# Optimization experiments

Hardware: AMD Instinct MI355X
Metric: run time of the kernel (lower is better)

Reference implementation:

```python
import jax, jax.numpy as jnp
import numpy as np

N_ITEMS = 100000
N_USERS = 16384
HIST = 50
TEXT_DIM = 256
GCN_DIM = 128
HIDDEN_DIM = 512
TOWER_DIM = 128


def _l2norm(x, eps=1e-12):
    # F.normalize(dim=1): x / max(||x||, eps)
    n = jnp.sqrt(jnp.sum(x * x, axis=1, keepdims=True))
    return x / jnp.maximum(n, eps)


def setup_inputs() -> dict:
    key = jax.random.key(0)
    ks = jax.random.split(key, 10)
    s1i = 1.0 / np.sqrt(TEXT_DIM + GCN_DIM)
    s2i = 1.0 / np.sqrt(HIDDEN_DIM)
    s1u = 1.0 / np.sqrt(GCN_DIM + TOWER_DIM)
    return {
        "item_text_emb": jax.random.normal(ks[0], (N_ITEMS, TEXT_DIM), jnp.float32),
        "gcn_item_emb": jax.random.normal(ks[1], (N_ITEMS, GCN_DIM), jnp.float32),
        "gcn_user_emb": jax.random.normal(ks[2], (N_USERS, GCN_DIM), jnp.float32),
        "hist_idx": jax.random.randint(ks[3], (N_USERS, HIST), 0, N_ITEMS),
        "W1i": jax.random.normal(ks[4], (TEXT_DIM + GCN_DIM, HIDDEN_DIM), jnp.float32) * s1i,
        "b1i": jnp.zeros((HIDDEN_DIM,), jnp.float32),
        "W2i": jax.random.normal(ks[5], (HIDDEN_DIM, TOWER_DIM), jnp.float32) * s2i,
        "b2i": jnp.zeros((TOWER_DIM,), jnp.float32),
        "W1u": jax.random.normal(ks[6], (GCN_DIM + TOWER_DIM, HIDDEN_DIM), jnp.float32) * s1u,
        "b1u": jnp.zeros((HIDDEN_DIM,), jnp.float32),
        "W2u": jax.random.normal(ks[7], (HIDDEN_DIM, TOWER_DIM), jnp.float32) * s2i,
        "b2u": jnp.zeros((TOWER_DIM,), jnp.float32),
    }


def reference(item_text_emb, gcn_item_emb, gcn_user_emb, hist_idx,
              W1i, b1i, W2i, b2i, W1u, b1u, W2u, b2u):
    # encode_items: MLP over concat(text, gcn) features, then L2 normalize
    item_feat = jnp.concatenate([item_text_emb, gcn_item_emb], axis=1)  # [N_items, text+gcn]
    h = jax.nn.relu(item_feat @ W1i + b1i)
    item_emb = _l2norm(h @ W2i + b2i)  # [N_items, TOWER_DIM]
    # encode_users: per-user gather of history item embeddings + mean pooling
    hist = jnp.mean(item_emb[hist_idx], axis=1)  # [N_users, TOWER_DIM]
    fused = jnp.concatenate([gcn_user_emb, hist], axis=1)
    hu = jax.nn.relu(fused @ W1u + b1u)
    user_emb = _l2norm(hu @ W2u + b2u)  # [N_users, TOWER_DIM]
    return user_emb
```

## Files before the change

kernel.cpp:

```cpp
#include <hip/hip_runtime.h>
#include <hip/hip_bf16.h>

#define HIST 50
#define N_ITEMS 100000
#define N_USERS 16384

typedef __bf16 bf8 __attribute__((ext_vector_type(8)));
typedef float  f4  __attribute__((ext_vector_type(4)));

__device__ __forceinline__ unsigned short f2bf(float x) {
    unsigned u = __builtin_bit_cast(unsigned, x);
    u += 0x7fffu + ((u >> 16) & 1u);
    return (unsigned short)(u >> 16);
}
__device__ __forceinline__ float bf2f(unsigned b) {
    unsigned u = b << 16;
    return __builtin_bit_cast(float, u);
}

__global__ void pack_weights(const float* __restrict__ W1i, const float* __restrict__ W2i,
                             const float* __restrict__ W1u, const float* __restrict__ W2u,
                             unsigned short* __restrict__ dstbase)
{
    int i = blockIdx.x * 256 + threadIdx.x;
    const float* W; unsigned short* dst; int N, KS, loc;
    if (i < 24576)      { W = W1i; dst = dstbase;          N = 512; KS = 12; loc = i; }
    else if (i < 32768) { W = W2i; dst = dstbase + 196608; N = 128; KS = 16; loc = i - 24576; }
    else if (i < 49152) { W = W1u; dst = dstbase + 262144; N = 512; KS = 8;  loc = i - 32768; }
    else                { W = W2u; dst = dstbase + 393216; N = 128; KS = 16; loc = i - 49152; }
    int l = loc & 63, fi = loc >> 6;
    int ks = fi % KS, nt = fi / KS;
    int q = l >> 4, c = l & 15;
    const float* src = W + (size_t)(ks * 32 + q * 8) * N + nt * 16 + c;
    unsigned o[4];
    #pragma unroll
    for (int k = 0; k < 4; ++k) {
        unsigned lo = f2bf(src[(2 * k) * N]);
        unsigned hi = f2bf(src[(2 * k + 1) * N]);
        o[k] = lo | (hi << 16);
    }
    uint4 v; v.x = o[0]; v.y = o[1]; v.z = o[2]; v.w = o[3];
    ((uint4*)dst)[(size_t)(nt * KS + ks) * 64 + l] = v;
}

template<int KS1, int ASTR, bool OUT_BF16>
__device__ __forceinline__ void tower_core(
    unsigned short* U, const float* b1s, const float* b2s, float* sumsq,
    const bf8* __restrict__ w1f, const bf8* __restrict__ w2f,
    void* __restrict__ outp, int row0, int tid)
{
    const int HSTR = 520;
    const int l = tid & 63, w = tid >> 6;
    const int q = l >> 4, c = l & 15;

    f4 acc1[2][4];
    #pragma unroll
    for (int i = 0; i < 2; ++i)
        #pragma unroll
        for (int j = 0; j < 4; ++j) acc1[i][j] = (f4)0.0f;

    const unsigned short* ap = U + c * ASTR + q * 8;
    #pragma unroll
    for (int ks = 0; ks < KS1; ++ks) {
        bf8 a0 = *(const bf8*)(ap + ks * 32);
        bf8 a1 = *(const bf8*)(ap + 16 * ASTR + ks * 32);
        #pragma unroll
        for (int nt = 0; nt < 4; ++nt) {
            bf8 b = w1f[(size_t)((w * 4 + nt) * KS1 + ks) * 64 + l];
            acc1[0][nt] = __builtin_amdgcn_mfma_f32_16x16x32_bf16(a0, b, acc1[0][nt], 0, 0, 0);
            acc1[1][nt] = __builtin_amdgcn_mfma_f32_16x16x32_bf16(a1, b, acc1[1][nt], 0, 0, 0);
        }
    }
    __syncthreads();

    #pragma unroll
    for (int nt = 0; nt < 4; ++nt) {
        int col = w * 64 + nt * 16 + c;
        float bias = b1s[col];
        #pragma unroll
        for (int rt = 0; rt < 2; ++rt)
            #pragma unroll
            for (int reg = 0; reg < 4; ++reg) {
                float h = fmaxf(acc1[rt][nt][reg] + bias, 0.0f);
                U[(rt * 16 + q * 4 + reg) * HSTR + col] = f2bf(h);
            }
    }
    __syncthreads();

    const int rg = w >> 2, jj = w & 3;
    f4 acc2[2];
    acc2[0] = (f4)0.0f; acc2[1] = (f4)0.0f;

    const unsigned short* hp = U + (size_t)(rg * 16 + c) * HSTR + q * 8;
    #pragma unroll
    for (int ks = 0; ks < 16; ++ks) {
        bf8 a = *(const bf8*)(hp + ks * 32);
        bf8 b0 = w2f[(size_t)((jj * 2 + 0) * 16 + ks) * 64 + l];
        bf8 b1 = w2f[(size_t)((jj * 2 + 1) * 16 + ks) * 64 + l];
        acc2[0] = __builtin_amdgcn_mfma_f32_16x16x32_bf16(a, b0, acc2[0], 0, 0, 0);
        acc2[1] = __builtin_amdgcn_mfma_f32_16x16x32_bf16(a, b1, acc2[1], 0, 0, 0);
    }

    float v[2][4];
    #pragma unroll
    for (int j = 0; j < 2; ++j) {
        float bias = b2s[jj * 32 + j * 16 + c];
        #pragma unroll
        for (int reg = 0; reg < 4; ++reg)
            v[j][reg] = acc2[j][reg] + bias;
    }
    #pragma unroll
    for (int reg = 0; reg < 4; ++reg) {
        float s = v[0][reg] * v[0][reg] + v[1][reg] * v[1][reg];
        s += __shfl_xor(s, 1); s += __shfl_xor(s, 2);
        s += __shfl_xor(s, 4); s += __shfl_xor(s, 8);
        if (c == 0) atomicAdd(&sumsq[rg * 16 + q * 4 + reg], s);
    }
    __syncthreads();
    #pragma unroll
    for (int reg = 0; reg < 4; ++reg) {
        int row = rg * 16 + q * 4 + reg;
        float inv = 1.0f / fmaxf(sqrtf(sumsq[row]), 1e-12f);
        #pragma unroll
        for (int j = 0; j < 2; ++j) {
            int col = jj * 32 + j * 16 + c;
            float o = v[j][reg] * inv;
            if (OUT_BF16)
                ((unsigned short*)outp)[(size_t)(row0 + row) * 128 + col] = f2bf(o);
            else
                ((float*)outp)[(size_t)(row0 + row) * 128 + col] = o;
        }
    }
}

#define ASI 392
#define ASU 264

__global__ __launch_bounds__(512, 8) void item_kernel(
    const float* __restrict__ text, const float* __restrict__ gcn,
    const bf8* __restrict__ w1f, const float* __restrict__ b1,
    const bf8* __restrict__ w2f, const float* __restrict__ b2,
    unsigned short* __restrict__ item_bf)
{
    __shared__ __align__(16) unsigned short U[32 * 520];
    __shared__ float b1s[512], b2s[128], sumsq[32];
    const int tid = threadIdx.x;
    const int row0 = blockIdx.x * 32;
    const float4* t4 = (const float4*)text;
    const float4* g4 = (const float4*)gcn;
    #pragma unroll
    for (int j = 0; j < 4; ++j) {
        int idx = tid + j * 512; int r = idx >> 6, c4 = idx & 63;
        float4 x = t4[(size_t)(row0 + r) * 64 + c4];
        ushort4 s; s.x = f2bf(x.x); s.y = f2bf(x.y); s.z = f2bf(x.z); s.w = f2bf(x.w);
        *(ushort4*)(U + r * ASI + c4 * 4) = s;
    }
    #pragma unroll
    for (int j = 0; j < 2; ++j) {
        int idx = tid + j * 512; int r = idx >> 5, c4 = idx & 31;
        float4 x = g4[(size_t)(row0 + r) * 32 + c4];
        ushort4 s; s.x = f2bf(x.x); s.y = f2bf(x.y); s.z = f2bf(x.z); s.w = f2bf(x.w);
        *(ushort4*)(U + r * ASI + 256 + c4 * 4) = s;
    }
    b1s[tid] = b1[tid];
    if (tid < 128) b2s[tid] = b2[tid];
    if (tid < 32)  sumsq[tid] = 0.0f;
    __syncthreads();
    tower_core<12, ASI, true>(U, b1s, b2s, sumsq, w1f, w2f, item_bf, row0, tid);
}

__global__ __launch_bounds__(512, 8) void user_kernel(
    const float* __restrict__ gcnu, const int* __restrict__ hist,
    const unsigned short* __restrict__ item_bf,
    const bf8* __restrict__ w1f, const float* __restrict__ b1,
    const bf8* __restrict__ w2f, const float* __restrict__ b2,
    float* __restrict__ outp)
{
    __shared__ __align__(16) unsigned short U[32 * 520];
    __shared__ float b1s[512], b2s[128], sumsq[32];
    const int tid = threadIdx.x;
    const int u0 = blockIdx.x * 32;
    int* hist_s = (int*)(U + 32 * ASU);
    const float4* g4 = (const float4*)gcnu;
    #pragma unroll
    for (int j = 0; j < 2; ++j) {
        int idx = tid + j * 512; int r = idx >> 5, c4 = idx & 31;
        float4 x = g4[(size_t)(u0 + r) * 32 + c4];
        ushort4 s; s.x = f2bf(x.x); s.y = f2bf(x.y); s.z = f2bf(x.z); s.w = f2bf(x.w);
        *(ushort4*)(U + r * ASU + c4 * 4) = s;
    }
    for (int k = tid; k < 32 * HIST; k += 512)
        hist_s[k] = hist[(size_t)u0 * HIST + k];
    b1s[tid] = b1[tid];
    if (tid < 128) b2s[tid] = b2[tid];
    if (tid < 32)  sumsq[tid] = 0.0f;
    __syncthreads();
    {
        const int u = tid >> 4, g = tid & 15;
        float f[8];
        #pragma unroll
        for (int k = 0; k < 8; ++k) f[k] = 0.0f;
        const int* hrow = hist_s + u * HIST;
        #pragma unroll 10
        for (int t = 0; t < HIST; ++t) {
            int id = hrow[t];
            uint4 x = *(const uint4*)(item_bf + (size_t)id * 128 + g * 8);
            unsigned vs[4] = {x.x, x.y, x.z, x.w};
            #pragma unroll
            for (int k = 0; k < 4; ++k) {
                f[2 * k]     += bf2f(vs[k] & 0xffffu);
                f[2 * k + 1] += bf2f(vs[k] >> 16);
            }
        }
        unsigned o[4];
        #pragma unroll
        for (int k = 0; k < 4; ++k)
            o[k] = (unsigned)f2bf(f[2 * k] * 0.02f) | ((unsigned)f2bf(f[2 * k + 1] * 0.02f) << 16);
        uint4 s; s.x = o[0]; s.y = o[1]; s.z = o[2]; s.w = o[3];
        *(uint4*)(U + u * ASU + 128 + g * 8) = s;
    }
    __syncthreads();
    tower_core<8, ASU, false>(U, b1s, b2s, sumsq, w1f, w2f, outp, u0, tid);
}

extern "C" void kernel_launch(void* const* d_in, const int* in_sizes, int n_in,
                              void* d_out, int out_size, void* d_ws, size_t ws_size,
                              hipStream_t stream) {
    const float* text = (const float*)d_in[0];
    const float* gcni = (const float*)d_in[1];
    const float* gcnu = (const float*)d_in[2];
    const int*   hist = (const int*)d_in[3];
    const float* W1i  = (const float*)d_in[4];
    const float* b1i  = (const float*)d_in[5];
    const float* W2i  = (const float*)d_in[6];
    const float* b2i  = (const float*)d_in[7];
    const float* W1u  = (const float*)d_in[8];
    const float* b1u  = (const float*)d_in[9];
    const float* W2u  = (const float*)d_in[10];
    const float* b2u  = (const float*)d_in[11];
    float* out = (float*)d_out;

    unsigned short* itemb = (unsigned short*)d_ws;
    unsigned short* pw = itemb + 12800000;

    pack_weights<<<224, 256, 0, stream>>>(W1i, W2i, W1u, W2u, pw);
    item_kernel<<<N_ITEMS / 32, 512, 0, stream>>>(
        text, gcni, (const bf8*)pw, b1i, (const bf8*)(pw + 196608), b2i, itemb);
    user_kernel<<<N_USERS / 32, 512, 0, stream>>>(
        gcnu, hist, itemb, (const bf8*)(pw + 262144), b1u, (const bf8*)(pw + 393216), b2u, out);
}
```

Before: 320.3 us.

## Double item tile to 64 rows, prefetch weight fragments, use nontemporal loads/stores

The item kernel now processes 64 rows per block instead of 32. Each weight fragment fetched from global memory is reused across four row tiles instead of two, which halves weight traffic per item. Weight fragments for the next k-step are software-prefetched into registers in both GEMM loops. Streaming inputs and outputs use nontemporal loads and stores, and a bounds guard covers the partial last tile. In exchange, the item kernel uses twice the shared memory, needs more accumulator registers, and the launch bound drops to 4 blocks per CU, which lowers occupancy.

Result: slower. 327.0 us (+2.1%).

```diff
diff --git a/kernel.cpp b/kernel.cpp
--- a/kernel.cpp
+++ b/kernel.cpp
@@ -7,6 +7,7 @@
 
 typedef __bf16 bf8 __attribute__((ext_vector_type(8)));
 typedef float  f4  __attribute__((ext_vector_type(4)));
+typedef float  f4v __attribute__((ext_vector_type(4)));
 
 __device__ __forceinline__ unsigned short f2bf(float x) {
     unsigned u = __builtin_bit_cast(unsigned, x);
@@ -43,33 +44,45 @@
     ((uint4*)dst)[(size_t)(nt * KS + ks) * 64 + l] = v;
 }
 
-template<int KS1, int ASTR, bool OUT_BF16>
+template<int NR, int KS1, int ASTR, bool OUT_BF16>
 __device__ __forceinline__ void tower_core(
     unsigned short* U, const float* b1s, const float* b2s, float* sumsq,
     const bf8* __restrict__ w1f, const bf8* __restrict__ w2f,
-    void* __restrict__ outp, int row0, int tid)
+    void* __restrict__ outp, int row0, int nval, int tid)
 {
     const int HSTR = 520;
     const int l = tid & 63, w = tid >> 6;
     const int q = l >> 4, c = l & 15;
 
-    f4 acc1[2][4];
-    #pragma unroll
-    for (int i = 0; i < 2; ++i)
+    f4 acc1[NR][4];
+    #pragma unroll
+    for (int i = 0; i < NR; ++i)
         #pragma unroll
         for (int j = 0; j < 4; ++j) acc1[i][j] = (f4)0.0f;
 
     const unsigned short* ap = U + c * ASTR + q * 8;
+    bf8 bcur[4], bnxt[4];
+    #pragma unroll
+    for (int nt = 0; nt < 4; ++nt)
+        bcur[nt] = w1f[(size_t)((w * 4 + nt) * KS1 + 0) * 64 + l];
     #pragma unroll
     for (int ks = 0; ks < KS1; ++ks) {
-        bf8 a0 = *(const bf8*)(ap + ks * 32);
-        bf8 a1 = *(const bf8*)(ap + 16 * ASTR + ks * 32);
-        #pragma unroll
-        for (int nt = 0; nt < 4; ++nt) {
-            bf8 b = w1f[(size_t)((w * 4 + nt) * KS1 + ks) * 64 + l];
-            acc1[0][nt] = __builtin_amdgcn_mfma_f32_16x16x32_bf16(a0, b, acc1[0][nt], 0, 0, 0);
-            acc1[1][nt] = __builtin_amdgcn_mfma_f32_16x16x32_bf16(a1, b, acc1[1][nt], 0, 0, 0);
-        }
+        if (ks + 1 < KS1) {
+            #pragma unroll
+            for (int nt = 0; nt < 4; ++nt)
+                bnxt[nt] = w1f[(size_t)((w * 4 + nt) * KS1 + ks + 1) * 64 + l];
+        }
+        bf8 a[NR];
+        #pragma unroll
+        for (int rt = 0; rt < NR; ++rt)
+            a[rt] = *(const bf8*)(ap + rt * 16 * ASTR + ks * 32);
+        #pragma unroll
+        for (int rt = 0; rt < NR; ++rt)
+            #pragma unroll
+            for (int nt = 0; nt < 4; ++nt)
+                acc1[rt][nt] = __builtin_amdgcn_mfma_f32_16x16x32_bf16(a[rt], bcur[nt], acc1[rt][nt], 0, 0, 0);
+        #pragma unroll
+        for (int nt = 0; nt < 4; ++nt) bcur[nt] = bnxt[nt];
     }
     __syncthreads();
 
@@ -78,7 +91,7 @@
         int col = w * 64 + nt * 16 + c;
         float bias = b1s[col];
         #pragma unroll
-        for (int rt = 0; rt < 2; ++rt)
+        for (int rt = 0; rt < NR; ++rt)
             #pragma unroll
             for (int reg = 0; reg < 4; ++reg) {
                 float h = fmaxf(acc1[rt][nt][reg] + bias, 0.0f);
@@ -87,89 +100,116 @@
     }
     __syncthreads();
 
+    constexpr int NR2 = NR / 2;
     const int rg = w >> 2, jj = w & 3;
-    f4 acc2[2];
-    acc2[0] = (f4)0.0f; acc2[1] = (f4)0.0f;
-
-    const unsigned short* hp = U + (size_t)(rg * 16 + c) * HSTR + q * 8;
+    f4 acc2[NR2][2];
+    #pragma unroll
+    for (int i = 0; i < NR2; ++i) { acc2[i][0] = (f4)0.0f; acc2[i][1] = (f4)0.0f; }
+
+    const unsigned short* hp = U + (size_t)(rg * NR2 * 16 + c) * HSTR + q * 8;
+    bf8 ccur[2], cnxt[2];
+    ccur[0] = w2f[(size_t)((jj * 2 + 0) * 16 + 0) * 64 + l];
+    ccur[1] = w2f[(size_t)((jj * 2 + 1) * 16 + 0) * 64 + l];
     #pragma unroll
     for (int ks = 0; ks < 16; ++ks) {
-        bf8 a = *(const bf8*)(hp + ks * 32);
-        bf8 b0 = w2f[(size_t)((jj * 2 + 0) * 16 + ks) * 64 + l];
-        bf8 b1 = w2f[(size_t)((jj * 2 + 1) * 16 + ks) * 64 + l];
-        acc2[0] = __builtin_amdgcn_mfma_f32_16x16x32_bf16(a, b0, acc2[0], 0, 0, 0);
-        acc2[1] = __builtin_amdgcn_mfma_f32_16x16x32_bf16(a, b1, acc2[1], 0, 0, 0);
-    }
-
-    float v[2][4];
-    #pragma unroll
-    for (int j = 0; j < 2; ++j) {
-        float bias = b2s[jj * 32 + j * 16 + c];
-        #pragma unroll
-        for (int reg = 0; reg < 4; ++reg)
-            v[j][reg] = acc2[j][reg] + bias;
-    }
-    #pragma unroll
-    for (int reg = 0; reg < 4; ++reg) {
-        float s = v[0][reg] * v[0][reg] + v[1][reg] * v[1][reg];
-        s += __shfl_xor(s, 1); s += __shfl_xor(s, 2);
-        s += __shfl_xor(s, 4); s += __shfl_xor(s, 8);
-        if (c == 0) atomicAdd(&sumsq[rg * 16 + q * 4 + reg], s);
-    }
-    __syncthreads();
-    #pragma unroll
-    for (int reg = 0; reg < 4; ++reg) {
-        int row = rg * 16 + q * 4 + reg;
-        float inv = 1.0f / fmaxf(sqrtf(sumsq[row]), 1e-12f);
+        if (ks + 1 < 16) {
+            cnxt[0] = w2f[(size_t)((jj * 2 + 0) * 16 + ks + 1) * 64 + l];
+            cnxt[1] = w2f[(size_t)((jj * 2 + 1) * 16 + ks + 1) * 64 + l];
+        }
+        bf8 a[NR2];
+        #pragma unroll
+        for (int i = 0; i < NR2; ++i)
+            a[i] = *(const bf8*)(hp + i * 16 * HSTR + ks * 32);
+        #pragma unroll
+        for (int i = 0; i < NR2; ++i) {
+            acc2[i][0] = __builtin_amdgcn_mfma_f32_16x16x32_bf16(a[i], ccur[0], acc2[i][0], 0, 0, 0);
+            acc2[i][1] = __builtin_amdgcn_mfma_f32_16x16x32_bf16(a[i], ccur[1], acc2[i][1], 0, 0, 0);
+        }
+        ccur[0] = cnxt[0]; ccur[1] = cnxt[1];
+    }
+
+    float v[NR2][2][4];
+    #pragma unroll
+    for (int i = 0; i < NR2; ++i)
         #pragma unroll
         for (int j = 0; j < 2; ++j) {
-            int col = jj * 32 + j * 16 + c;
-            float o = v[j][reg] * inv;
-            if (OUT_BF16)
-                ((unsigned short*)outp)[(size_t)(row0 + row) * 128 + col] = f2bf(o);
-            else
-                ((float*)outp)[(size_t)(row0 + row) * 128 + col] = o;
-        }
-    }
+            float bias = b2s[jj * 32 + j * 16 + c];
+            #pragma unroll
+            for (int reg = 0; reg < 4; ++reg)
+                v[i][j][reg] = acc2[i][j][reg] + bias;
+        }
+    #pragma unroll
+    for (int i = 0; i < NR2; ++i)
+        #pragma unroll
+        for (int reg = 0; reg < 4; ++reg) {
+            float s = v[i][0][reg] * v[i][0][reg] + v[i][1][reg] * v[i][1][reg];
+            s += __shfl_xor(s, 1); s += __shfl_xor(s, 2);
+            s += __shfl_xor(s, 4); s += __shfl_xor(s, 8);
+            if (c == 0) atomicAdd(&sumsq[rg * NR2 * 16 + i * 16 + q * 4 + reg], s);
+        }
+    __syncthreads();
+    #pragma unroll
+    for (int i = 0; i < NR2; ++i)
+        #pragma unroll
+        for (int reg = 0; reg < 4; ++reg) {
+            int row = rg * NR2 * 16 + i * 16 + q * 4 + reg;
+            if (row < nval) {
+                float inv = 1.0f / fmaxf(sqrtf(sumsq[row]), 1e-12f);
+                #pragma unroll
+                for (int j = 0; j < 2; ++j) {
+                    int col = jj * 32 + j * 16 + c;
+                    float o = v[i][j][reg] * inv;
+                    if (OUT_BF16)
+                        __builtin_nontemporal_store(f2bf(o),
+                            ((unsigned short*)outp) + (size_t)(row0 + row) * 128 + col);
+                    else
+                        __builtin_nontemporal_store(o,
+                            ((float*)outp) + (size_t)(row0 + row) * 128 + col);
+                }
+            }
+        }
 }
 
 #define ASI 392
 #define ASU 264
 
-__global__ __launch_bounds__(512, 8) void item_kernel(
+__global__ __launch_bounds__(512, 4) void item_kernel(
     const float* __restrict__ text, const float* __restrict__ gcn,
     const bf8* __restrict__ w1f, const float* __restrict__ b1,
     const bf8* __restrict__ w2f, const float* __restrict__ b2,
     unsigned short* __restrict__ item_bf)
 {
-    __shared__ __align__(16) unsigned short U[32 * 520];
-    __shared__ float b1s[512], b2s[128], sumsq[32];
+    __shared__ __align__(16) unsigned short U[64 * 520];
+    __shared__ float b1s[512], b2s[128], sumsq[64];
     const int tid = threadIdx.x;
-    const int row0 = blockIdx.x * 32;
-    const float4* t4 = (const float4*)text;
-    const float4* g4 = (const float4*)gcn;
+    const int row0 = blockIdx.x * 64;
+    const int nval = min(64, N_ITEMS - row0);
+    const f4v* t4 = (const f4v*)text;
+    const f4v* g4 = (const f4v*)gcn;
+    #pragma unroll
+    for (int j = 0; j < 8; ++j) {
+        int idx = tid + j * 512; int r = idx >> 6, c4 = idx & 63;
+        f4v x = (r < nval) ? __builtin_nontemporal_load(t4 + (size_t)(row0 + r) * 64 + c4)
+                           : (f4v)0.0f;
+        ushort4 s; s.x = f2bf(x[0]); s.y = f2bf(x[1]); s.z = f2bf(x[2]); s.w = f2bf(x[3]);
+        *(ushort4*)(U + r * ASI + c4 * 4) = s;
+    }
     #pragma unroll
     for (int j = 0; j < 4; ++j) {
-        int idx = tid + j * 512; int r = idx >> 6, c4 = idx & 63;
-        float4 x = t4[(size_t)(row0 + r) * 64 + c4];
-        ushort4 s; s.x = f2bf(x.x); s.y = f2bf(x.y); s.z = f2bf(x.z); s.w = f2bf(x.w);
-        *(ushort4*)(U + r * ASI + c4 * 4) = s;
-    }
-    #pragma unroll
-    for (int j = 0; j < 2; ++j) {
         int idx = tid + j * 512; int r = idx >> 5, c4 = idx & 31;
-        float4 x = g4[(size_t)(row0 + r) * 32 + c4];
-        ushort4 s; s.x = f2bf(x.x); s.y = f2bf(x.y); s.z = f2bf(x.z); s.w = f2bf(x.w);
+        f4v x = (r < nval) ? __builtin_nontemporal_load(g4 + (size_t)(row0 + r) * 32 + c4)
+                           : (f4v)0.0f;
+        ushort4 s; s.x = f2bf(x[0]); s.y = f2bf(x[1]); s.z = f2bf(x[2]); s.w = f2bf(x[3]);
         *(ushort4*)(U + r * ASI + 256 + c4 * 4) = s;
     }
     b1s[tid] = b1[tid];
     if (tid < 128) b2s[tid] = b2[tid];
-    if (tid < 32)  sumsq[tid] = 0.0f;
-    __syncthreads();
-    tower_core<12, ASI, true>(U, b1s, b2s, sumsq, w1f, w2f, item_bf, row0, tid);
-}
-
-__global__ __launch_bounds__(512, 8) void user_kernel(
+    if (tid < 64)  sumsq[tid] = 0.0f;
+    __syncthreads();
+    tower_core<4, 12, ASI, true>(U, b1s, b2s, sumsq, w1f, w2f, item_bf, row0, nval, tid);
+}
+
+__global__ __launch_bounds__(512, 4) void user_kernel(
     const float* __restrict__ gcnu, const int* __restrict__ hist,
     const unsigned short* __restrict__ item_bf,
     const bf8* __restrict__ w1f, const float* __restrict__ b1,
@@ -181,16 +221,16 @@
     const int tid = threadIdx.x;
     const int u0 = blockIdx.x * 32;
     int* hist_s = (int*)(U + 32 * ASU);
-    const float4* g4 = (const float4*)gcnu;
+    const f4v* g4 = (const f4v*)gcnu;
     #pragma unroll
     for (int j = 0; j < 2; ++j) {
         int idx = tid + j * 512; int r = idx >> 5, c4 = idx & 31;
-        float4 x = g4[(size_t)(u0 + r) * 32 + c4];
-        ushort4 s; s.x = f2bf(x.x); s.y = f2bf(x.y); s.z = f2bf(x.z); s.w = f2bf(x.w);
+        f4v x = __builtin_nontemporal_load(g4 + (size_t)(u0 + r) * 32 + c4);
+        ushort4 s; s.x = f2bf(x[0]); s.y = f2bf(x[1]); s.z = f2bf(x[2]); s.w = f2bf(x[3]);
         *(ushort4*)(U + r * ASU + c4 * 4) = s;
     }
     for (int k = tid; k < 32 * HIST; k += 512)
-        hist_s[k] = hist[(size_t)u0 * HIST + k];
+        hist_s[k] = __builtin_nontemporal_load(hist + (size_t)u0 * HIST + k);
     b1s[tid] = b1[tid];
     if (tid < 128) b2s[tid] = b2[tid];
     if (tid < 32)  sumsq[tid] = 0.0f;
@@ -220,7 +260,7 @@
         *(uint4*)(U + u * ASU + 128 + g * 8) = s;
     }
     __syncthreads();
-    tower_core<8, ASU, false>(U, b1s, b2s, sumsq, w1f, w2f, outp, u0, tid);
+    tower_core<2, 8, ASU, false>(U, b1s, b2s, sumsq, w1f, w2f, outp, u0, 32, tid);
 }
 
 extern "C" void kernel_launch(void* const* d_in, const int* in_sizes, int n_in,
@@ -244,7 +284,7 @@
     unsigned short* pw = itemb + 12800000;
 
     pack_weights<<<224, 256, 0, stream>>>(W1i, W2i, W1u, W2u, pw);
-    item_kernel<<<N_ITEMS / 32, 512, 0, stream>>>(
+    item_kernel<<<(N_ITEMS + 63) / 64, 512, 0, stream>>>(
         text, gcni, (const bf8*)pw, b1i, (const bf8*)(pw + 196608), b2i, itemb);
     user_kernel<<<N_USERS / 32, 512, 0, stream>>>(
         gcnu, hist, itemb, (const bf8*)(pw + 262144), b1u, (const bf8*)(pw + 393216), b2u, out);
```
